# Kernel tuning notes

Hardware: AMD Instinct MI355X
Metric: run time of the kernel (lower is better)

The kernel has to match this reference:

```python
import jax, jax.numpy as jnp
import numpy as np
import math

B, N, M, H = 4, 1024, 1024, 512
EPS = 1e-5


def _ln(x, g, b):
    m = jnp.mean(x, axis=-1, keepdims=True)
    v = jnp.mean((x - m) ** 2, axis=-1, keepdims=True)
    return (x - m) * jax.lax.rsqrt(v + EPS) * g + b


def _heads(x, h):
    b, s, Hh = x.shape
    return x.reshape(b, s, h, Hh // h).transpose(0, 2, 1, 3)  # [b,h,s,d]


def _merge(x):
    b, h, s, d = x.shape
    return x.transpose(0, 2, 1, 3).reshape(b, s, h * d)


def _sdpa(q, k, v):
    d = q.shape[-1]
    a = jax.nn.softmax(jnp.einsum('bhqd,bhkd->bhqk', q, k) / math.sqrt(d), axis=-1)
    return jnp.einsum('bhqk,bhkd->bhqd', a, v)


def _attn(key, value, query, Wk, Wv, Wq, Wf, bf, g, b, h):
    residual = query
    K = _heads(key @ Wk, h)
    V = _heads(value @ Wv, h)
    Q = _heads(query @ Wq, h)
    r = _merge(_sdpa(Q, K, V))
    r = jnp.concatenate([residual, r], axis=-1) @ Wf + bf
    return _ln(r + residual, g, b)


def _sc_attn(x, x2, Wk, Wv, Wq, Wf, bf, g, b, h=2):
    residual = x
    sK, sV, sQ = _heads(x @ Wk, h), _heads(x @ Wv, h), _heads(x @ Wq, h)
    cK, cV, cQ = _heads(x2 @ Wk, h), _heads(x2 @ Wv, h), _heads(x2 @ Wq, h)
    r = _sdpa(sQ, sK, sV) + _sdpa(cQ, cK, cV) + _sdpa(cQ, sK, sV) + _sdpa(sQ, cK, cV)
    r = _merge(r)
    r = jnp.concatenate([residual, r], axis=-1) @ Wf + bf
    return _ln(r + residual, g, b)


def _forward(context_x, context_y, target_x, in_W, in_b, cx_W, cx_b, tx_W, tx_b,
             sc_Wk, sc_Wv, sc_Wq, sc_Wf, sc_bf, sc_g, sc_b,
             ca_Wk, ca_Wv, ca_Wq, ca_Wf, ca_bf, ca_g, ca_b):
    bsz = context_x.shape[0]
    y = context_y.reshape(bsz, -1, 4, 2)
    proj = lambda yd: jnp.concatenate([context_x, yd], axis=-1) @ in_W + in_b
    e = proj(y[:, :, 0, :])
    e1 = proj(y[:, :, 1, :])
    e2 = proj(y[:, :, 2, :])
    e3 = proj(y[:, :, 3, :])
    # first self pass: key2/value2/query2 == current encoder_input
    for i in range(2):
        e = _sc_attn(e, e, sc_Wk[i], sc_Wv[i], sc_Wq[i], sc_Wf[i], sc_bf[i], sc_g[i], sc_b[i])
    for x2 in (e1, e2, e3):
        for i in range(2):
            e = _sc_attn(e, x2, sc_Wk[i], sc_Wv[i], sc_Wq[i], sc_Wf[i], sc_bf[i], sc_g[i], sc_b[i])
    q = target_x @ tx_W + tx_b
    k = context_x @ cx_W + cx_b
    for i in range(2):
        q = _attn(k, e, q, ca_Wk[i], ca_Wv[i], ca_Wq[i], ca_Wf[i], ca_bf[i], ca_g[i], ca_b[i], h=4)
    return q


def setup_inputs() -> dict:
    key = jax.random.key(0)
    ks = jax.random.split(key, 24)
    w = lambda i, shape, s: jax.random.normal(ks[i], shape, jnp.float32) * s
    return {
        'context_x': jax.random.normal(ks[0], (B, N, 1), jnp.float32),
        'context_y': jax.random.normal(ks[1], (B, N, 8), jnp.float32),
        'target_x': jax.random.normal(ks[2], (B, M, 1), jnp.float32),
        'in_W': w(3, (3, H), 0.5), 'in_b': jnp.zeros((H,), jnp.float32),
        'cx_W': w(4, (1, H), 0.5), 'cx_b': jnp.zeros((H,), jnp.float32),
        'tx_W': w(5, (1, H), 0.5), 'tx_b': jnp.zeros((H,), jnp.float32),
        'sc_Wk': w(6, (2, H, H), 0.03), 'sc_Wv': w(7, (2, H, H), 0.03), 'sc_Wq': w(8, (2, H, H), 0.03),
        'sc_Wf': w(9, (2, 2 * H, H), 0.03), 'sc_bf': jnp.zeros((2, H), jnp.float32),
        'sc_g': jnp.ones((2, H), jnp.float32), 'sc_b': jnp.zeros((2, H), jnp.float32),
        'ca_Wk': w(10, (2, H, H), 0.03), 'ca_Wv': w(11, (2, H, H), 0.03), 'ca_Wq': w(12, (2, H, H), 0.03),
        'ca_Wf': w(13, (2, 2 * H, H), 0.03), 'ca_bf': jnp.zeros((2, H), jnp.float32),
        'ca_g': jnp.ones((2, H), jnp.float32), 'ca_b': jnp.zeros((2, H), jnp.float32),
    }


def reference(context_x, context_y, target_x, in_W, in_b, cx_W, cx_b, tx_W, tx_b,
              sc_Wk, sc_Wv, sc_Wq, sc_Wf, sc_bf, sc_g, sc_b,
              ca_Wk, ca_Wv, ca_Wq, ca_Wf, ca_bf, ca_g, ca_b):
    return _forward(context_x, context_y, target_x, in_W, in_b, cx_W, cx_b, tx_W, tx_b,
                    sc_Wk, sc_Wv, sc_Wq, sc_Wf, sc_bf, sc_g, sc_b,
                    ca_Wk, ca_Wv, ca_Wq, ca_Wf, ca_bf, ca_g, ca_b)
```

## Files before the change

### kernel.cpp

```cpp
#include <hip/hip_runtime.h>

#define DEVINL __device__ __forceinline__

typedef short bf16x8 __attribute__((ext_vector_type(8)));
typedef float f32x4 __attribute__((ext_vector_type(4)));

DEVINL unsigned f2b(float f) {
  unsigned u = __float_as_uint(f);
  u = (u + 0x7FFFu + ((u >> 16) & 1u)) >> 16;
  return u & 0xFFFFu;
}
DEVINL uint4 pack8(const float* v) {
  uint4 u;
  u.x = f2b(v[0]) | (f2b(v[1]) << 16);
  u.y = f2b(v[2]) | (f2b(v[3]) << 16);
  u.z = f2b(v[4]) | (f2b(v[5]) << 16);
  u.w = f2b(v[6]) | (f2b(v[7]) << 16);
  return u;
}

DEVINL float4 block_sum4(float4 v, float4* sh) {
  const int lane = threadIdx.x & 63, wid = threadIdx.x >> 6;
#pragma unroll
  for (int o = 32; o; o >>= 1) {
    v.x += __shfl_down(v.x, o);
    v.y += __shfl_down(v.y, o);
    v.z += __shfl_down(v.z, o);
    v.w += __shfl_down(v.w, o);
  }
  __syncthreads();
  if (lane == 0) sh[wid] = v;
  __syncthreads();
  float4 a = sh[0], b = sh[1], c = sh[2], d = sh[3], r;
  r.x = a.x + b.x + c.x + d.x;
  r.y = a.y + b.y + c.y + d.y;
  r.z = a.z + b.z + c.z + d.z;
  r.w = a.w + b.w + c.w + d.w;
  return r;
}
DEVINL float block_sum1(float v, float* sh) {
  const int lane = threadIdx.x & 63, wid = threadIdx.x >> 6;
#pragma unroll
  for (int o = 32; o; o >>= 1) v += __shfl_down(v, o);
  __syncthreads();
  if (lane == 0) sh[wid] = v;
  __syncthreads();
  return sh[0] + sh[1] + sh[2] + sh[3];
}

__global__ __launch_bounds__(256) void tabproj9_kernel(
    const float* __restrict__ in_W, const float* __restrict__ in_b,
    const float* __restrict__ cx_W, const float* __restrict__ cx_b,
    const float* __restrict__ tx_W, const float* __restrict__ tx_b,
    const float* __restrict__ sWk, const float* __restrict__ sWv,
    const float* __restrict__ sWq, const float* __restrict__ aWk,
    const float* __restrict__ aWq, float* __restrict__ Ttab) {
  const int z = blockIdx.y;
  const float* V;
  const float* bias;
  const float* W;
  float* P;
  int nvec;
  float scl = 1.f;
  if (z < 6) {
    V = in_W; bias = in_b; nvec = 3;
    const int i = z / 3, wsel = z % 3;
    W = (wsel == 0 ? sWk : wsel == 1 ? sWv : sWq) + (size_t)i * 262144;
    P = Ttab + (size_t)z * 2048;
    if (wsel == 2) scl = 0.0625f;
  } else if (z < 8) {
    V = cx_W; bias = cx_b; nvec = 1;
    W = aWk + (size_t)(z - 6) * 262144;
    P = Ttab + 12288 + (size_t)(z - 6) * 1024;
  } else {
    V = tx_W; bias = tx_b; nvec = 1;
    W = aWq; P = Ttab + 14336; scl = 0.08838834764831845f;
  }
  __shared__ float4 sh4[4];
  const int j = blockIdx.x, tid = threadIdx.x;
  float acc[4] = {0.f, 0.f, 0.f, 0.f};
  for (int kk = tid; kk < 512; kk += 256) {
    const float w = W[(size_t)kk * 512 + j];
    for (int v = 0; v < nvec; ++v) acc[v] += V[(size_t)v * 512 + kk] * w;
    acc[3] += bias[kk] * w;
  }
  float4 packed = make_float4(acc[0], acc[1], acc[2], acc[3]);
  packed = block_sum4(packed, sh4);
  if (tid == 0) {
    const float vals[4] = {packed.x * scl, packed.y * scl, packed.z * scl, packed.w * scl};
    for (int v = 0; v < nvec; ++v) P[(size_t)v * 512 + j] = vals[v];
    P[(size_t)nvec * 512 + j] = vals[3];
  }
}

__global__ __launch_bounds__(256) void transpose_kvq_kernel(
    const float* __restrict__ sWk, const float* __restrict__ sWv,
    const float* __restrict__ sWq, const float* __restrict__ aWv,
    const float* __restrict__ aWq, unsigned short* __restrict__ Wkvqt0,
    unsigned short* __restrict__ aWvt0, unsigned short* __restrict__ aWqt1) {
  const int z = blockIdx.z;
  const float* src;
  unsigned short* dst;
  float scl = 1.f;
  if (z < 6) {
    const int i = z / 3, wsel = z % 3;
    src = (wsel == 0 ? sWk : wsel == 1 ? sWv : sWq) + (size_t)i * 262144;
    dst = Wkvqt0 + (size_t)i * 786432 + (size_t)wsel * 262144;
    if (wsel == 2) scl = 0.0625f;
  } else if (z < 8) {
    src = aWv + (size_t)(z - 6) * 262144;
    dst = aWvt0 + (size_t)(z - 6) * 262144;
  } else {
    src = aWq + 262144; dst = aWqt1; scl = 0.08838834764831845f;
  }
  __shared__ float tile[32][33];
  const int n0 = blockIdx.x * 32, k0 = blockIdx.y * 32;
  const int tx = threadIdx.x, ty = threadIdx.y;
#pragma unroll
  for (int r = 0; r < 4; ++r)
    tile[ty + 8 * r][tx] = src[(size_t)(k0 + ty + 8 * r) * 512 + n0 + tx];
  __syncthreads();
#pragma unroll
  for (int r = 0; r < 4; ++r)
    dst[(size_t)(n0 + ty + 8 * r) * 512 + k0 + tx] =
        (unsigned short)f2b(scl * tile[tx][ty + 8 * r]);
}

__global__ __launch_bounds__(256) void transpose_f_kernel(
    const float* __restrict__ sWf, const float* __restrict__ aWf,
    unsigned short* __restrict__ Wft0, unsigned short* __restrict__ aWft0) {
  const int z = blockIdx.z;
  const float* src = (z < 2 ? sWf + (size_t)z * 524288 : aWf + (size_t)(z - 2) * 524288);
  unsigned short* dst =
      (z < 2 ? Wft0 + (size_t)z * 524288 : aWft0 + (size_t)(z - 2) * 524288);
  __shared__ float tile[32][33];
  const int n0 = blockIdx.x * 32, k0 = blockIdx.y * 32;
  const int tx = threadIdx.x, ty = threadIdx.y;
#pragma unroll
  for (int r = 0; r < 4; ++r)
    tile[ty + 8 * r][tx] = src[(size_t)(k0 + ty + 8 * r) * 512 + n0 + tx];
  __syncthreads();
#pragma unroll
  for (int r = 0; r < 4; ++r)
    dst[(size_t)(n0 + ty + 8 * r) * 1024 + k0 + tx] =
        (unsigned short)f2b(tile[tx][ty + 8 * r]);
}

__global__ __launch_bounds__(256) void vtrans_frag_kernel(
    const float* __restrict__ V, int ld, int nh, int D,
    unsigned short* __restrict__ Vfr) {
  __shared__ float tile[32][33];
  const int s0 = blockIdx.x * 32, d0 = blockIdx.y * 32;
  const int bh = blockIdx.z;
  const int b = bh / nh, h = bh % nh;
  const int tx = threadIdx.x, ty = threadIdx.y;
  const float* src = V + ((size_t)b * 1024 + s0) * ld + h * D + d0;
#pragma unroll
  for (int r = 0; r < 4; ++r)
    tile[ty + 8 * r][tx] = src[(size_t)(ty + 8 * r) * ld + tx];
  __syncthreads();
  const int idx = ty * 32 + tx;
  if (idx < 128) {
    const int dj = idx & 31, sch = idx >> 5;
    float v[8];
#pragma unroll
    for (int jj = 0; jj < 8; ++jj) v[jj] = tile[sch * 8 + jj][dj];
    const uint4 u = pack8(v);
    const int sc = s0 >> 5;
    const int dtile = (d0 + dj) >> 4;
    const int lane = sch * 16 + (dj & 15);
    *(uint4*)(Vfr + ((size_t)(bh * 32 + sc) * (D / 16) + dtile) * 512 + lane * 8) = u;
  }
}

__global__ __launch_bounds__(256) void affine3_pack_kernel(
    const float* __restrict__ cx, const float* __restrict__ cy, int sel,
    const float* __restrict__ TK, const float* __restrict__ TV,
    const float* __restrict__ TQ, unsigned short* __restrict__ Kfr,
    unsigned short* __restrict__ Qbf, float* __restrict__ Vf) {
  const int row = blockIdx.x;
  const int b = row >> 10, s = row & 1023;
  const float x = cx[row];
  const float* y = cy + (size_t)row * 8 + 2 * sel;
  const float y0 = y[0], y1 = y[1];
  const int t = threadIdx.x;
  if (t < 128) {
    const bool isQ = t >= 64;
    const int c = t & 63;
    const int h = c >> 5;
    const int d0 = (c & 31) * 8;
    const float* T = isQ ? TQ : TK;
    float v[8];
#pragma unroll
    for (int j = 0; j < 8; ++j) {
      const int col = h * 256 + d0 + j;
      v[j] = x * T[col] + y0 * T[512 + col] + y1 * T[1024 + col] + T[1536 + col];
    }
    const uint4 u = pack8(v);
    const int bh = b * 2 + h;
    if (isQ) {
      *(uint4*)(Qbf + ((size_t)bh * 1024 + s) * 256 + d0) = u;
    } else {
      const int kc = d0 >> 5;
      const int lane = ((d0 & 31) >> 3) * 16 + (s & 15);
      *(uint4*)(Kfr + ((size_t)(bh * 8 + kc) * 64 + (s >> 4)) * 512 + lane * 8) = u;
    }
  } else {
    const int col0 = (t - 128) * 4;
    float4 o;
    float* op = (float*)&o;
#pragma unroll
    for (int j = 0; j < 4; ++j) {
      const int col = col0 + j;
      op[j] = x * TV[col] + y0 * TV[512 + col] + y1 * TV[1024 + col] + TV[1536 + col];
    }
    *(float4*)(Vf + (size_t)row * 512 + col0) = o;
  }
}

__global__ __launch_bounds__(64) void rank1_pack_kernel(
    const float* __restrict__ x, const float* __restrict__ T,
    unsigned short* __restrict__ dst, int isQ) {
  const int row = blockIdx.x;
  const int b = row >> 10, s = row & 1023;
  const float xv = x[row];
  const int c = threadIdx.x;
  const int h = c >> 4;
  const int d0 = (c & 15) * 8;
  float v[8];
#pragma unroll
  for (int j = 0; j < 8; ++j) {
    const int col = h * 128 + d0 + j;
    v[j] = xv * T[col] + T[512 + col];
  }
  const uint4 u = pack8(v);
  const int bh = b * 4 + h;
  if (isQ) {
    *(uint4*)(dst + ((size_t)bh * 1024 + s) * 128 + d0) = u;
  } else {
    const int kc = d0 >> 5;
    const int lane = ((d0 & 31) >> 3) * 16 + (s & 15);
    *(uint4*)(dst + ((size_t)(bh * 4 + kc) * 64 + (s >> 4)) * 512 + lane * 8) = u;
  }
}

__global__ __launch_bounds__(512) void affine3_kernel(
    const float* __restrict__ cx, const float* __restrict__ cy, int sel,
    const float* __restrict__ W3, const float* __restrict__ bias,
    float* __restrict__ out, unsigned short* __restrict__ outb) {
  const int r = blockIdx.x, j = threadIdx.x;
  const float* y = cy + (size_t)r * 8 + 2 * sel;
  const float v = cx[r] * W3[j] + y[0] * W3[512 + j] + y[1] * W3[1024 + j] + bias[j];
  if (out) out[(size_t)r * 512 + j] = v;
  if (outb) outb[(size_t)r * 512 + j] = (unsigned short)f2b(v);
}

__global__ __launch_bounds__(512) void rank1_kernel(
    const float* __restrict__ x, const float* __restrict__ w,
    const float* __restrict__ b, float* __restrict__ out,
    unsigned short* __restrict__ outb) {
  const int r = blockIdx.x, j = threadIdx.x;
  const float v = x[r] * w[j] + b[j];
  if (out) out[(size_t)r * 512 + j] = v;
  if (outb) outb[(size_t)r * 512 + j] = (unsigned short)f2b(v);
}

__global__ __launch_bounds__(256) void gemm_wf_kernel(
    const unsigned short* __restrict__ A0, const unsigned short* __restrict__ A1,
    const float* __restrict__ F0, const float* __restrict__ F1,
    const unsigned short* __restrict__ Wt, const float* __restrict__ bias,
    float* __restrict__ C0, float* __restrict__ C1) {
  constexpr int BM = 128, BN = 64, BK = 32, LDP = 40, K = 512, N = 512;
  __shared__ unsigned short As[2][BM * LDP];
  __shared__ unsigned short Bs[2][BN * LDP];
  const int kz = blockIdx.z;
  const int tid = threadIdx.x;
  const int lane = tid & 63, w = tid >> 6;
  const int bm = blockIdx.y * BM, bn = blockIdx.x * BN;
  const int wm = (w & 1) * 64, wn = (w >> 1) * 32;
  const int l15 = lane & 15, lq = lane >> 4;
  const int ar = tid >> 1, ac = (tid & 1) * 16;
  const int br = tid >> 2, bc = (tid & 3) * 8;
  const unsigned short* A = kz ? A1 : A0;
  const bool useF = (kz != 0) && (F0 != nullptr);
  const size_t arow = (size_t)(bm + ar) * 512;
  const size_t brow = (size_t)(bn + br) * 1024 + (size_t)kz * 512;
  f32x4 acc[4][2] = {};
  uint4 ra0, ra1, rb0;
#define GLOAD(k0_)                                                          \
  do {                                                                      \
    if (useF) {                                                             \
      const float* p0 = F0 + arow + (k0_) + ac;                             \
      const float* p1 = F1 + arow + (k0_) + ac;                             \
      float s[16];                                                          \
      const float4 x0 = *(const float4*)p0, x1 = *(const float4*)(p0 + 4);  \
      const float4 x2 = *(const float4*)(p0 + 8), x3 = *(const float4*)(p0 + 12); \
      const float4 y0 = *(const float4*)p1, y1 = *(const float4*)(p1 + 4);  \
      const float4 y2 = *(const float4*)(p1 + 8), y3 = *(const float4*)(p1 + 12); \
      s[0] = x0.x + y0.x; s[1] = x0.y + y0.y; s[2] = x0.z + y0.z; s[3] = x0.w + y0.w; \
      s[4] = x1.x + y1.x; s[5] = x1.y + y1.y; s[6] = x1.z + y1.z; s[7] = x1.w + y1.w; \
      s[8] = x2.x + y2.x; s[9] = x2.y + y2.y; s[10] = x2.z + y2.z; s[11] = x2.w + y2.w; \
      s[12] = x3.x + y3.x; s[13] = x3.y + y3.y; s[14] = x3.z + y3.z; s[15] = x3.w + y3.w; \
      ra0 = pack8(s); ra1 = pack8(s + 8);                                   \
    } else {                                                                \
      ra0 = *(const uint4*)(A + arow + (k0_) + ac);                         \
      ra1 = *(const uint4*)(A + arow + (k0_) + ac + 8);                     \
    }                                                                       \
    rb0 = *(const uint4*)(Wt + brow + (k0_) + bc);                          \
  } while (0)
  GLOAD(0);
  *(uint4*)(As[0] + ar * LDP + ac) = ra0;
  *(uint4*)(As[0] + ar * LDP + ac + 8) = ra1;
  *(uint4*)(Bs[0] + br * LDP + bc) = rb0;
  __syncthreads();
  int buf = 0;
  for (int k0 = 0; k0 < K; k0 += BK) {
    const bool more = (k0 + BK) < K;
    if (more) GLOAD(k0 + BK);
    bf16x8 af[4], bfr[2];
#pragma unroll
    for (int mt = 0; mt < 4; ++mt)
      af[mt] = *(const bf16x8*)(As[buf] + (wm + mt * 16 + l15) * LDP + lq * 8);
#pragma unroll
    for (int nt = 0; nt < 2; ++nt)
      bfr[nt] = *(const bf16x8*)(Bs[buf] + (wn + nt * 16 + l15) * LDP + lq * 8);
#pragma unroll
    for (int mt = 0; mt < 4; ++mt)
#pragma unroll
      for (int nt = 0; nt < 2; ++nt)
        acc[mt][nt] =
            __builtin_amdgcn_mfma_f32_16x16x32_bf16(af[mt], bfr[nt], acc[mt][nt], 0, 0, 0);
    if (more) {
      *(uint4*)(As[buf ^ 1] + ar * LDP + ac) = ra0;
      *(uint4*)(As[buf ^ 1] + ar * LDP + ac + 8) = ra1;
      *(uint4*)(Bs[buf ^ 1] + br * LDP + bc) = rb0;
    }
    __syncthreads();
    buf ^= 1;
  }
#undef GLOAD
  float* C = kz ? C1 : C0;
#pragma unroll
  for (int nt = 0; nt < 2; ++nt) {
    const int col = bn + wn + nt * 16 + l15;
    const float bv = (kz && bias) ? bias[col] : 0.f;
#pragma unroll
    for (int mt = 0; mt < 4; ++mt) {
#pragma unroll
      for (int r = 0; r < 4; ++r) {
        const int row = bm + wm + mt * 16 + lq * 4 + r;
        C[(size_t)row * N + col] = acc[mt][nt][r] + bv;
      }
    }
  }
}

template <int MODE>
__global__ __launch_bounds__(256) void gemm_pack_kernel(
    const unsigned short* __restrict__ A0, const unsigned short* __restrict__ Wt,
    unsigned short* __restrict__ Kfr, unsigned short* __restrict__ Vfr,
    unsigned short* __restrict__ Qbf) {
  constexpr int BM = 128, BN = 64, BK = 32, LDP = 40, K = 512;
  __shared__ unsigned short As[2][BM * LDP];
  __shared__ unsigned short Bs[2][BN * LDP];
  const int tid = threadIdx.x;
  const int lane = tid & 63, w = tid >> 6;
  const int bm = blockIdx.y * BM, bn = blockIdx.x * BN;
  const int wm = (w & 1) * 64, wn = (w >> 1) * 32;
  const int l15 = lane & 15, lq = lane >> 4;
  const int ar = tid >> 1, ac = (tid & 1) * 16;
  const int br = tid >> 2, bc = (tid & 3) * 8;
  f32x4 acc[4][2] = {};
  uint4 ra0 = *(const uint4*)(A0 + (size_t)(bm + ar) * K + ac);
  uint4 ra1 = *(const uint4*)(A0 + (size_t)(bm + ar) * K + ac + 8);
  uint4 rb0 = *(const uint4*)(Wt + (size_t)(bn + br) * K + bc);
  *(uint4*)(As[0] + ar * LDP + ac) = ra0;
  *(uint4*)(As[0] + ar * LDP + ac + 8) = ra1;
  *(uint4*)(Bs[0] + br * LDP + bc) = rb0;
  __syncthreads();
  int buf = 0;
  for (int k0 = 0; k0 < K; k0 += BK) {
    const bool more = (k0 + BK) < K;
    if (more) {
      ra0 = *(const uint4*)(A0 + (size_t)(bm + ar) * K + k0 + BK + ac);
      ra1 = *(const uint4*)(A0 + (size_t)(bm + ar) * K + k0 + BK + ac + 8);
      rb0 = *(const uint4*)(Wt + (size_t)(bn + br) * K + k0 + BK + bc);
    }
    bf16x8 af[4], bfr[2];
#pragma unroll
    for (int mt = 0; mt < 4; ++mt)
      af[mt] = *(const bf16x8*)(As[buf] + (wm + mt * 16 + l15) * LDP + lq * 8);
#pragma unroll
    for (int nt = 0; nt < 2; ++nt)
      bfr[nt] = *(const bf16x8*)(Bs[buf] + (wn + nt * 16 + l15) * LDP + lq * 8);
#pragma unroll
    for (int mt = 0; mt < 4; ++mt)
#pragma unroll
      for (int nt = 0; nt < 2; ++nt)
        acc[mt][nt] =
            __builtin_amdgcn_mfma_f32_16x16x32_bf16(af[mt], bfr[nt], acc[mt][nt], 0, 0, 0);
    if (more) {
      *(uint4*)(As[buf ^ 1] + ar * LDP + ac) = ra0;
      *(uint4*)(As[buf ^ 1] + ar * LDP + ac + 8) = ra1;
      *(uint4*)(Bs[buf ^ 1] + br * LDP + bc) = rb0;
    }
    __syncthreads();
    buf ^= 1;
  }
  const int b = bm >> 10;
  const int s0base = (bm & 1023) + wm + lq * 4;
#pragma unroll
  for (int nt = 0; nt < 2; ++nt) {
    const int col = bn + wn + nt * 16 + l15;
    int sec, h, d, nh2, Dv;
    if constexpr (MODE == 0) {
      sec = col >> 9; const int c = col & 511; h = c >> 8; d = c & 255; nh2 = 2; Dv = 256;
    } else if constexpr (MODE == 1) {
      sec = 1; h = col >> 7; d = col & 127; nh2 = 4; Dv = 128;
    } else {
      sec = 2; h = col >> 7; d = col & 127; nh2 = 4; Dv = 128;
    }
    const int bh = b * nh2 + h;
#pragma unroll
    for (int mt = 0; mt < 4; ++mt) {
      const int s0 = s0base + mt * 16;
      const float* a = (const float*)&acc[mt][nt];
      if (sec == 2) {
        unsigned short* q = Qbf + ((size_t)bh * 1024 + s0) * Dv + d;
#pragma unroll
        for (int r = 0; r < 4; ++r) q[(size_t)r * Dv] = (unsigned short)f2b(a[r]);
      } else if (sec == 0) {
        unsigned short* kp = Kfr +
            ((size_t)(bh * 8 + (d >> 5)) * 64 + (s0 >> 4)) * 512 +
            ((d & 31) >> 3) * 128 + (d & 7);
#pragma unroll
        for (int r = 0; r < 4; ++r)
          kp[((s0 & 15) + r) * 8] = (unsigned short)f2b(a[r]);
      } else {
        unsigned short* vp = Vfr +
            ((size_t)(bh * 32 + (s0 >> 5)) * (Dv / 16) + (d >> 4)) * 512 +
            (((s0 >> 3) & 3) * 16 + (d & 15)) * 8 + (s0 & 7);
        uint2 u;
        u.x = f2b(a[0]) | (f2b(a[1]) << 16);
        u.y = f2b(a[2]) | (f2b(a[3]) << 16);
        *(uint2*)vp = u;
      }
    }
  }
}

template <int D, int NKV>
__global__ __launch_bounds__(256, 2) void attn_mfma_kernel(
    const unsigned short* __restrict__ Qa, const unsigned short* __restrict__ Qb,
    const unsigned short* __restrict__ KfrA, const unsigned short* __restrict__ KfrB,
    const unsigned short* __restrict__ VfrA, const unsigned short* __restrict__ VfrB,
    float post_scale, int nh, unsigned short* __restrict__ R,
    float* __restrict__ Rp) {
  constexpr int NQS = NKV;
  constexpr int QP = D + 8;
  constexpr int WP = 1024 + 8;
  constexpr int DT = D / 64;
  const int tid = threadIdx.x;
  const int lane = tid & 63, w = tid >> 6;
  const int l15 = lane & 15, lq = lane >> 4;
  const int nbh = 4 * nh;
  int bx = blockIdx.x;
  int side = 0;
  if constexpr (NKV == 2) { side = bx >> 9; bx &= 511; }
  const int bh = bx % nbh;
  const int qb16 = (bx / nbh) * 16;
  const int b = bh / nh, head = bh % nh;
  const size_t rowb = (size_t)b * 1024;
  const int colo = head * D;

  __shared__ unsigned short qsh[NQS * 16 * QP];
  __shared__ unsigned short wsh[16 * WP];
  __shared__ float redA[4][16];
  __shared__ float redB[4][16];

  for (int idx = tid; idx < NQS * 16 * (D / 8); idx += 256) {
    const int st = idx / (16 * (D / 8));
    const int rem = idx - st * 16 * (D / 8);
    const int r = rem / (D / 8), ch = rem - r * (D / 8);
    const unsigned short* Q = st ? Qb : Qa;
    const uint4 u = *(const uint4*)(Q + ((size_t)bh * 1024 + qb16 + r) * D + ch * 8);
    *(uint4*)(qsh + st * 16 * QP + r * QP + ch * 8) = u;
  }
  __syncthreads();

  const unsigned short* Kp = (side ? KfrB : KfrA) + (size_t)bh * ((size_t)D * 1024);
  const unsigned short* Vp = (side ? VfrB : VfrA) + (size_t)bh * ((size_t)D * 1024);

  f32x4 acc[NQS][16] = {};
#pragma unroll 1
  for (int kc = 0; kc < D / 32; ++kc) {
    bf16x8 kf[16];
#pragma unroll
    for (int st = 0; st < 16; ++st)
      kf[st] = *(const bf16x8*)(Kp + ((size_t)kc * 64 + w * 16 + st) * 512 + lane * 8);
    const bf16x8 qa = *(const bf16x8*)(qsh + l15 * QP + kc * 32 + lq * 8);
    __builtin_amdgcn_s_setprio(1);
#pragma unroll
    for (int st = 0; st < 16; ++st)
      acc[0][st] = __builtin_amdgcn_mfma_f32_16x16x32_bf16(qa, kf[st], acc[0][st], 0, 0, 0);
    __builtin_amdgcn_s_setprio(0);
    if constexpr (NQS == 2) {
      const bf16x8 qb2 = *(const bf16x8*)(qsh + 16 * QP + l15 * QP + kc * 32 + lq * 8);
      __builtin_amdgcn_s_setprio(1);
#pragma unroll
      for (int st = 0; st < 16; ++st)
        acc[1][st] =
            __builtin_amdgcn_mfma_f32_16x16x32_bf16(qb2, kf[st], acc[1][st], 0, 0, 0);
      __builtin_amdgcn_s_setprio(0);
    }
  }

  float psA[4] = {0.f, 0.f, 0.f, 0.f}, psB[4] = {0.f, 0.f, 0.f, 0.f};
#pragma unroll
  for (int st = 0; st < 16; ++st)
#pragma unroll
    for (int r = 0; r < 4; ++r) {
      acc[0][st][r] = __expf(acc[0][st][r]);
      psA[r] += acc[0][st][r];
      if constexpr (NQS == 2) {
        acc[1][st][r] = __expf(acc[1][st][r]);
        psB[r] += acc[1][st][r];
      }
    }
#pragma unroll
  for (int o = 1; o < 16; o <<= 1)
#pragma unroll
    for (int r = 0; r < 4; ++r) {
      psA[r] += __shfl_xor(psA[r], o);
      if constexpr (NQS == 2) psB[r] += __shfl_xor(psB[r], o);
    }
  if (l15 == 0) {
#pragma unroll
    for (int r = 0; r < 4; ++r) {
      redA[w][lq * 4 + r] = psA[r];
      if constexpr (NQS == 2) redB[w][lq * 4 + r] = psB[r];
    }
  }
  __syncthreads();
  float invA[4], invB[4];
#pragma unroll
  for (int r = 0; r < 4; ++r) {
    invA[r] = 1.f / (redA[0][lq * 4 + r] + redA[1][lq * 4 + r] +
                     redA[2][lq * 4 + r] + redA[3][lq * 4 + r]);
    if constexpr (NQS == 2)
      invB[r] = 1.f / (redB[0][lq * 4 + r] + redB[1][lq * 4 + r] +
                       redB[2][lq * 4 + r] + redB[3][lq * 4 + r]);
  }
#pragma unroll
  for (int st = 0; st < 16; ++st)
#pragma unroll
    for (int r = 0; r < 4; ++r) {
      float wv = acc[0][st][r] * invA[r];
      if constexpr (NQS == 2) wv += acc[1][st][r] * invB[r];
      wsh[(lq * 4 + r) * WP + w * 256 + st * 16 + l15] = (unsigned short)f2b(wv);
    }
  __syncthreads();

  f32x4 acc_o[DT] = {};
#pragma unroll 1
  for (int sc = 0; sc < 32; sc += 2) {
    bf16x8 pa[2], vb[2][DT];
#pragma unroll
    for (int u = 0; u < 2; ++u) {
      pa[u] = *(const bf16x8*)(wsh + l15 * WP + (sc + u) * 32 + lq * 8);
#pragma unroll
      for (int dt = 0; dt < DT; ++dt)
        vb[u][dt] = *(const bf16x8*)(
            Vp + ((size_t)(sc + u) * (D / 16) + w * DT + dt) * 512 + lane * 8);
    }
    __builtin_amdgcn_s_setprio(1);
#pragma unroll
    for (int u = 0; u < 2; ++u)
#pragma unroll
      for (int dt = 0; dt < DT; ++dt)
        acc_o[dt] =
            __builtin_amdgcn_mfma_f32_16x16x32_bf16(pa[u], vb[u][dt], acc_o[dt], 0, 0, 0);
    __builtin_amdgcn_s_setprio(0);
  }

  if constexpr (NKV == 2) {
    float* dst = Rp + (size_t)side * (4096 * 512) + (rowb + qb16) * 512 + colo;
#pragma unroll
    for (int dt = 0; dt < DT; ++dt)
#pragma unroll
      for (int r = 0; r < 4; ++r) {
        const int q = lq * 4 + r;
        const int d = w * (DT * 16) + dt * 16 + l15;
        dst[(size_t)q * 512 + d] = acc_o[dt][r];
      }
  } else {
#pragma unroll
    for (int dt = 0; dt < DT; ++dt)
#pragma unroll
      for (int r = 0; r < 4; ++r) {
        const int q = lq * 4 + r;
        const int d = w * (DT * 16) + dt * 16 + l15;
        R[(rowb + qb16 + q) * 512 + colo + d] =
            (unsigned short)f2b(acc_o[dt][r] * post_scale);
      }
  }
}

__global__ __launch_bounds__(256) void ln_kernel(
    const float* __restrict__ G0, const float* __restrict__ G1,
    const float* __restrict__ res, const float* __restrict__ g,
    const float* __restrict__ b, float* __restrict__ out,
    unsigned short* __restrict__ outb) {
  __shared__ float sh[4];
  const int row = blockIdx.x, tid = threadIdx.x;
  const size_t off = (size_t)row * 512;
  const float x0 = G0[off + tid] + G1[off + tid] + res[off + tid];
  const float x1 = G0[off + tid + 256] + G1[off + tid + 256] + res[off + tid + 256];
  const float mean = block_sum1(x0 + x1, sh) * (1.0f / 512.0f);
  const float d0 = x0 - mean, d1 = x1 - mean;
  const float var = block_sum1(d0 * d0 + d1 * d1, sh) * (1.0f / 512.0f);
  const float inv = rsqrtf(var + 1e-5f);
  const float y0 = d0 * inv * g[tid] + b[tid];
  const float y1 = d1 * inv * g[tid + 256] + b[tid + 256];
  out[off + tid] = y0;
  out[off + tid + 256] = y1;
  if (outb) {
    outb[off + tid] = (unsigned short)f2b(y0);
    outb[off + tid + 256] = (unsigned short)f2b(y1);
  }
}

extern "C" void kernel_launch(void* const* d_in, const int* in_sizes, int n_in,
                              void* d_out, int out_size, void* d_ws, size_t ws_size,
                              hipStream_t stream) {
  typedef unsigned short ushort_t;
  const float* cx   = (const float*)d_in[0];
  const float* cy   = (const float*)d_in[1];
  const float* txp  = (const float*)d_in[2];
  const float* in_W = (const float*)d_in[3];
  const float* in_b = (const float*)d_in[4];
  const float* cx_W = (const float*)d_in[5];
  const float* cx_b = (const float*)d_in[6];
  const float* tx_W = (const float*)d_in[7];
  const float* tx_b = (const float*)d_in[8];
  const float* sWk  = (const float*)d_in[9];
  const float* sWv  = (const float*)d_in[10];
  const float* sWq  = (const float*)d_in[11];
  const float* sWf  = (const float*)d_in[12];
  const float* sbf  = (const float*)d_in[13];
  const float* sg   = (const float*)d_in[14];
  const float* sb   = (const float*)d_in[15];
  const float* aWk  = (const float*)d_in[16];
  const float* aWv  = (const float*)d_in[17];
  const float* aWq  = (const float*)d_in[18];
  const float* aWf  = (const float*)d_in[19];
  const float* abf  = (const float*)d_in[20];
  const float* ag   = (const float*)d_in[21];
  const float* ab   = (const float*)d_in[22];

  const size_t MB = 1024 * 1024;
  char* ws = (char*)d_ws;
  float*    E     = (float*)(ws + 0 * MB);
  ushort_t* Ebf   = (ushort_t*)(ws + 8 * MB);
  float*    QA    = (float*)(ws + 12 * MB);
  ushort_t* QAbf  = (ushort_t*)(ws + 20 * MB);
  ushort_t* Rbbf  = (ushort_t*)(ws + 24 * MB);
  float*    Rp    = (float*)(ws + 28 * MB);
  float*    G0    = (float*)(ws + 44 * MB);
  ushort_t* KfrA  = (ushort_t*)(ws + 52 * MB);
  ushort_t* VfrA  = (ushort_t*)(ws + 56 * MB);
  ushort_t* QbfA  = (ushort_t*)(ws + 60 * MB);
  ushort_t* KfrB  = (ushort_t*)(ws + 64 * MB);
  ushort_t* VfrB  = (ushort_t*)(ws + 68 * MB);
  ushort_t* QbfB  = (ushort_t*)(ws + 72 * MB);
  float*    cVf   = (float*)(ws + 76 * MB);
  float*    G1    = (float*)(ws + 84 * MB);
  ushort_t* Wkvqt0 = (ushort_t*)(ws + 92 * MB);
  ushort_t* Wkvqt[2] = {Wkvqt0, Wkvqt0 + 786432};
  ushort_t* Wft0   = (ushort_t*)(ws + 95 * MB);
  ushort_t* Wft[2] = {Wft0, Wft0 + 524288};
  ushort_t* aWvt0  = (ushort_t*)(ws + 97 * MB);
  ushort_t* aWvt[2] = {aWvt0, aWvt0 + 262144};
  ushort_t* aWqt1  = (ushort_t*)(ws + 98 * MB);
  ushort_t* aWft0  = (ushort_t*)(ws + 99 * MB);
  ushort_t* aWft[2] = {aWft0, aWft0 + 524288};
  float*    Ttab   = (float*)(ws + 101 * MB);

  float* T_sc[2][3];
  for (int i = 0; i < 2; ++i)
    for (int w = 0; w < 3; ++w) T_sc[i][w] = Ttab + (size_t)(i * 3 + w) * 2048;
  float* T_cak[2] = {Ttab + 12288, Ttab + 12288 + 1024};
  float* T_caq0 = Ttab + 14336;

  const dim3 tb(32, 8);

  transpose_kvq_kernel<<<dim3(16, 16, 9), tb, 0, stream>>>(sWk, sWv, sWq, aWv, aWq,
                                                           Wkvqt0, aWvt0, aWqt1);
  transpose_f_kernel<<<dim3(16, 32, 4), tb, 0, stream>>>(sWf, aWf, Wft0, aWft0);
  tabproj9_kernel<<<dim3(512, 9), 256, 0, stream>>>(in_W, in_b, cx_W, cx_b, tx_W, tx_b,
                                                    sWk, sWv, sWq, aWk, aWq, Ttab);

  affine3_kernel<<<4096, 512, 0, stream>>>(cx, cy, 0, in_W, in_b, E, Ebf);
  rank1_kernel<<<4096, 512, 0, stream>>>(txp, tx_W, tx_b, QA, QAbf);

  for (int p = 0; p < 4; ++p) {
    for (int i = 0; i < 2; ++i) {
      gemm_pack_kernel<0><<<dim3(24, 32), 256, 0, stream>>>(Ebf, Wkvqt[i], KfrA, VfrA,
                                                            QbfA);
      const float* F0 = nullptr;
      const float* F1 = nullptr;
      if (p > 0) {
        affine3_pack_kernel<<<4096, 256, 0, stream>>>(cx, cy, p, T_sc[i][0], T_sc[i][1],
                                                      T_sc[i][2], KfrB, QbfB, cVf);
        vtrans_frag_kernel<<<dim3(32, 8, 8), tb, 0, stream>>>(cVf, 512, 2, 256, VfrB);
        attn_mfma_kernel<256, 2><<<1024, 256, 0, stream>>>(
            QbfA, QbfB, KfrA, KfrB, VfrA, VfrB, 1.0f, 2, nullptr, Rp);
        F0 = Rp; F1 = Rp + 4096 * 512;
      } else {
        attn_mfma_kernel<256, 1><<<512, 256, 0, stream>>>(
            QbfA, QbfA, KfrA, KfrA, VfrA, VfrA, 4.0f, 2, Rbbf, nullptr);
      }
      gemm_wf_kernel<<<dim3(8, 32, 2), 256, 0, stream>>>(
          Ebf, Rbbf, F0, F1, Wft[i], sbf + (size_t)i * 512, G0, G1);
      ln_kernel<<<4096, 256, 0, stream>>>(G0, G1, E, sg + (size_t)i * 512,
                                          sb + (size_t)i * 512, E, Ebf);
    }
  }

  for (int i = 0; i < 2; ++i) {
    rank1_pack_kernel<<<4096, 64, 0, stream>>>(cx, T_cak[i], KfrA, 0);
    gemm_pack_kernel<1><<<dim3(8, 32), 256, 0, stream>>>(Ebf, aWvt[i], nullptr, VfrA,
                                                         nullptr);
    if (i == 0) {
      rank1_pack_kernel<<<4096, 64, 0, stream>>>(txp, T_caq0, QbfB, 1);
    } else {
      gemm_pack_kernel<2><<<dim3(8, 32), 256, 0, stream>>>(QAbf, aWqt1, nullptr, nullptr,
                                                           QbfB);
    }
    attn_mfma_kernel<128, 1><<<1024, 256, 0, stream>>>(
        QbfB, QbfB, KfrA, KfrA, VfrA, VfrA, 1.0f, 4, Rbbf, nullptr);
    gemm_wf_kernel<<<dim3(8, 32, 2), 256, 0, stream>>>(
        QAbf, Rbbf, nullptr, nullptr, aWft[i], abf + (size_t)i * 512, G0, G1);
    ln_kernel<<<4096, 256, 0, stream>>>(G0, G1, QA, ag + (size_t)i * 512,
                                        ab + (size_t)i * 512,
                                        (i == 1) ? (float*)d_out : QA,
                                        (i == 1) ? nullptr : QAbf);
  }
  (void)in_sizes; (void)n_in; (void)out_size; (void)ws_size;
}
```

Baseline: 1.060 ms.

## Fuse V affine into fragment packing, use exp2 softmax, halve attention weight smem

Folds log2(e) into the Q scaling so the softmax can use exp2f instead of __expf. Replaces the affine3_pack plus vtrans_frag pair with a K/Q affine kernel and a V kernel that computes the affine values directly into the fragment layout, which removes the fp32 V intermediate round-trip through global memory. The attention kernel now stages probability weights through half-sized shared memory in two passes. That lowers LDS use and may raise occupancy, but adds extra barriers and a remapped V chunk index.

Measured after the change: 1.592 ms. +50.2%, slower.

```diff
diff --git a/kernel.cpp b/kernel.cpp
--- a/kernel.cpp
+++ b/kernel.cpp
@@ -4,6 +4,8 @@
 
 typedef short bf16x8 __attribute__((ext_vector_type(8)));
 typedef float f32x4 __attribute__((ext_vector_type(4)));
+
+#define LOG2E 1.44269504088896f
 
 DEVINL unsigned f2b(float f) {
   unsigned u = __float_as_uint(f);
@@ -67,14 +69,14 @@
     const int i = z / 3, wsel = z % 3;
     W = (wsel == 0 ? sWk : wsel == 1 ? sWv : sWq) + (size_t)i * 262144;
     P = Ttab + (size_t)z * 2048;
-    if (wsel == 2) scl = 0.0625f;
+    if (wsel == 2) scl = 0.0625f * LOG2E;
   } else if (z < 8) {
     V = cx_W; bias = cx_b; nvec = 1;
     W = aWk + (size_t)(z - 6) * 262144;
     P = Ttab + 12288 + (size_t)(z - 6) * 1024;
   } else {
     V = tx_W; bias = tx_b; nvec = 1;
-    W = aWq; P = Ttab + 14336; scl = 0.08838834764831845f;
+    W = aWq; P = Ttab + 14336; scl = 0.08838834764831845f * LOG2E;
   }
   __shared__ float4 sh4[4];
   const int j = blockIdx.x, tid = threadIdx.x;
@@ -106,12 +108,12 @@
     const int i = z / 3, wsel = z % 3;
     src = (wsel == 0 ? sWk : wsel == 1 ? sWv : sWq) + (size_t)i * 262144;
     dst = Wkvqt0 + (size_t)i * 786432 + (size_t)wsel * 262144;
-    if (wsel == 2) scl = 0.0625f;
+    if (wsel == 2) scl = 0.0625f * LOG2E;
   } else if (z < 8) {
     src = aWv + (size_t)(z - 6) * 262144;
     dst = aWvt0 + (size_t)(z - 6) * 262144;
   } else {
-    src = aWq + 262144; dst = aWqt1; scl = 0.08838834764831845f;
+    src = aWq + 262144; dst = aWqt1; scl = 0.08838834764831845f * LOG2E;
   }
   __shared__ float tile[32][33];
   const int n0 = blockIdx.x * 32, k0 = blockIdx.y * 32;
@@ -146,75 +148,68 @@
         (unsigned short)f2b(tile[tx][ty + 8 * r]);
 }
 
-__global__ __launch_bounds__(256) void vtrans_frag_kernel(
-    const float* __restrict__ V, int ld, int nh, int D,
-    unsigned short* __restrict__ Vfr) {
-  __shared__ float tile[32][33];
-  const int s0 = blockIdx.x * 32, d0 = blockIdx.y * 32;
-  const int bh = blockIdx.z;
-  const int b = bh / nh, h = bh % nh;
-  const int tx = threadIdx.x, ty = threadIdx.y;
-  const float* src = V + ((size_t)b * 1024 + s0) * ld + h * D + d0;
-#pragma unroll
-  for (int r = 0; r < 4; ++r)
-    tile[ty + 8 * r][tx] = src[(size_t)(ty + 8 * r) * ld + tx];
-  __syncthreads();
-  const int idx = ty * 32 + tx;
-  if (idx < 128) {
-    const int dj = idx & 31, sch = idx >> 5;
-    float v[8];
-#pragma unroll
-    for (int jj = 0; jj < 8; ++jj) v[jj] = tile[sch * 8 + jj][dj];
-    const uint4 u = pack8(v);
-    const int sc = s0 >> 5;
-    const int dtile = (d0 + dj) >> 4;
-    const int lane = sch * 16 + (dj & 15);
-    *(uint4*)(Vfr + ((size_t)(bh * 32 + sc) * (D / 16) + dtile) * 512 + lane * 8) = u;
-  }
-}
-
-__global__ __launch_bounds__(256) void affine3_pack_kernel(
+__global__ __launch_bounds__(128) void affine3kq_kernel(
     const float* __restrict__ cx, const float* __restrict__ cy, int sel,
-    const float* __restrict__ TK, const float* __restrict__ TV,
-    const float* __restrict__ TQ, unsigned short* __restrict__ Kfr,
-    unsigned short* __restrict__ Qbf, float* __restrict__ Vf) {
+    const float* __restrict__ TK, const float* __restrict__ TQ,
+    unsigned short* __restrict__ Kfr, unsigned short* __restrict__ Qbf) {
   const int row = blockIdx.x;
   const int b = row >> 10, s = row & 1023;
   const float x = cx[row];
   const float* y = cy + (size_t)row * 8 + 2 * sel;
   const float y0 = y[0], y1 = y[1];
   const int t = threadIdx.x;
-  if (t < 128) {
-    const bool isQ = t >= 64;
-    const int c = t & 63;
-    const int h = c >> 5;
-    const int d0 = (c & 31) * 8;
-    const float* T = isQ ? TQ : TK;
+  const bool isQ = t >= 64;
+  const int c = t & 63;
+  const int h = c >> 5;
+  const int d0 = (c & 31) * 8;
+  const float* T = isQ ? TQ : TK;
+  float v[8];
+#pragma unroll
+  for (int j = 0; j < 8; ++j) {
+    const int col = h * 256 + d0 + j;
+    v[j] = x * T[col] + y0 * T[512 + col] + y1 * T[1024 + col] + T[1536 + col];
+  }
+  const uint4 u = pack8(v);
+  const int bh = b * 2 + h;
+  if (isQ) {
+    *(uint4*)(Qbf + ((size_t)bh * 1024 + s) * 256 + d0) = u;
+  } else {
+    const int kc = d0 >> 5;
+    const int lane = ((d0 & 31) >> 3) * 16 + (s & 15);
+    *(uint4*)(Kfr + ((size_t)(bh * 8 + kc) * 64 + (s >> 4)) * 512 + lane * 8) = u;
+  }
+}
+
+__global__ __launch_bounds__(256) void affine3v_frag_kernel(
+    const float* __restrict__ cx, const float* __restrict__ cy, int sel,
+    const float* __restrict__ TV, unsigned short* __restrict__ Vfr) {
+  __shared__ float tile[32][33];
+  const int s0 = blockIdx.x * 32, d0 = blockIdx.y * 32;
+  const int bh = blockIdx.z;
+  const int b = bh >> 1, h = bh & 1;
+  const int tx = threadIdx.x, ty = threadIdx.y;
+  const int col = h * 256 + d0 + tx;
+  const float tv0 = TV[col], tv1 = TV[512 + col], tv2 = TV[1024 + col],
+              tv3 = TV[1536 + col];
+#pragma unroll
+  for (int r = 0; r < 4; ++r) {
+    const int row = b * 1024 + s0 + ty + 8 * r;
+    const float x = cx[row];
+    const float* y = cy + (size_t)row * 8 + 2 * sel;
+    tile[ty + 8 * r][tx] = x * tv0 + y[0] * tv1 + y[1] * tv2 + tv3;
+  }
+  __syncthreads();
+  const int idx = ty * 32 + tx;
+  if (idx < 128) {
+    const int dj = idx & 31, sch = idx >> 5;
     float v[8];
 #pragma unroll
-    for (int j = 0; j < 8; ++j) {
-      const int col = h * 256 + d0 + j;
-      v[j] = x * T[col] + y0 * T[512 + col] + y1 * T[1024 + col] + T[1536 + col];
-    }
+    for (int jj = 0; jj < 8; ++jj) v[jj] = tile[sch * 8 + jj][dj];
     const uint4 u = pack8(v);
-    const int bh = b * 2 + h;
-    if (isQ) {
-      *(uint4*)(Qbf + ((size_t)bh * 1024 + s) * 256 + d0) = u;
-    } else {
-      const int kc = d0 >> 5;
-      const int lane = ((d0 & 31) >> 3) * 16 + (s & 15);
-      *(uint4*)(Kfr + ((size_t)(bh * 8 + kc) * 64 + (s >> 4)) * 512 + lane * 8) = u;
-    }
-  } else {
-    const int col0 = (t - 128) * 4;
-    float4 o;
-    float* op = (float*)&o;
-#pragma unroll
-    for (int j = 0; j < 4; ++j) {
-      const int col = col0 + j;
-      op[j] = x * TV[col] + y0 * TV[512 + col] + y1 * TV[1024 + col] + TV[1536 + col];
-    }
-    *(float4*)(Vf + (size_t)row * 512 + col0) = o;
+    const int sc = s0 >> 5;
+    const int dtile = (d0 + dj) >> 4;
+    const int lane = sch * 16 + (dj & 15);
+    *(uint4*)(Vfr + ((size_t)(bh * 32 + sc) * 16 + dtile) * 512 + lane * 8) = u;
   }
 }
 
@@ -458,7 +453,7 @@
     float* __restrict__ Rp) {
   constexpr int NQS = NKV;
   constexpr int QP = D + 8;
-  constexpr int WP = 1024 + 8;
+  constexpr int WPh = 512 + 8;
   constexpr int DT = D / 64;
   const int tid = threadIdx.x;
   const int lane = tid & 63, w = tid >> 6;
@@ -474,7 +469,7 @@
   const int colo = head * D;
 
   __shared__ unsigned short qsh[NQS * 16 * QP];
-  __shared__ unsigned short wsh[16 * WP];
+  __shared__ unsigned short wsh[16 * WPh];
   __shared__ float redA[4][16];
   __shared__ float redB[4][16];
 
@@ -520,10 +515,10 @@
   for (int st = 0; st < 16; ++st)
 #pragma unroll
     for (int r = 0; r < 4; ++r) {
-      acc[0][st][r] = __expf(acc[0][st][r]);
+      acc[0][st][r] = exp2f(acc[0][st][r]);
       psA[r] += acc[0][st][r];
       if constexpr (NQS == 2) {
-        acc[1][st][r] = __expf(acc[1][st][r]);
+        acc[1][st][r] = exp2f(acc[1][st][r]);
         psB[r] += acc[1][st][r];
       }
     }
@@ -551,36 +546,44 @@
       invB[r] = 1.f / (redB[0][lq * 4 + r] + redB[1][lq * 4 + r] +
                        redB[2][lq * 4 + r] + redB[3][lq * 4 + r]);
   }
-#pragma unroll
-  for (int st = 0; st < 16; ++st)
-#pragma unroll
-    for (int r = 0; r < 4; ++r) {
-      float wv = acc[0][st][r] * invA[r];
-      if constexpr (NQS == 2) wv += acc[1][st][r] * invB[r];
-      wsh[(lq * 4 + r) * WP + w * 256 + st * 16 + l15] = (unsigned short)f2b(wv);
-    }
-  __syncthreads();
 
   f32x4 acc_o[DT] = {};
 #pragma unroll 1
-  for (int sc = 0; sc < 32; sc += 2) {
-    bf16x8 pa[2], vb[2][DT];
-#pragma unroll
-    for (int u = 0; u < 2; ++u) {
-      pa[u] = *(const bf16x8*)(wsh + l15 * WP + (sc + u) * 32 + lq * 8);
-#pragma unroll
-      for (int dt = 0; dt < DT; ++dt)
-        vb[u][dt] = *(const bf16x8*)(
-            Vp + ((size_t)(sc + u) * (D / 16) + w * DT + dt) * 512 + lane * 8);
-    }
-    __builtin_amdgcn_s_setprio(1);
-#pragma unroll
-    for (int u = 0; u < 2; ++u)
-#pragma unroll
-      for (int dt = 0; dt < DT; ++dt)
-        acc_o[dt] =
-            __builtin_amdgcn_mfma_f32_16x16x32_bf16(pa[u], vb[u][dt], acc_o[dt], 0, 0, 0);
-    __builtin_amdgcn_s_setprio(0);
+  for (int half = 0; half < 2; ++half) {
+#pragma unroll
+    for (int st = 0; st < 8; ++st) {
+      const int g = half * 8 + st;
+#pragma unroll
+      for (int r = 0; r < 4; ++r) {
+        float wv = acc[0][g][r] * invA[r];
+        if constexpr (NQS == 2) wv += acc[1][g][r] * invB[r];
+        wsh[(lq * 4 + r) * WPh + w * 128 + st * 16 + l15] = (unsigned short)f2b(wv);
+      }
+    }
+    __syncthreads();
+#pragma unroll 1
+    for (int sh2 = 0; sh2 < 16; sh2 += 2) {
+      bf16x8 pa[2], vb[2][DT];
+#pragma unroll
+      for (int u = 0; u < 2; ++u) {
+        const int sc = sh2 + u;
+        pa[u] = *(const bf16x8*)(wsh + l15 * WPh + sc * 32 + lq * 8);
+        const int scg = (sc >> 2) * 8 + half * 4 + (sc & 3);
+#pragma unroll
+        for (int dt = 0; dt < DT; ++dt)
+          vb[u][dt] = *(const bf16x8*)(
+              Vp + ((size_t)scg * (D / 16) + w * DT + dt) * 512 + lane * 8);
+      }
+      __builtin_amdgcn_s_setprio(1);
+#pragma unroll
+      for (int u = 0; u < 2; ++u)
+#pragma unroll
+        for (int dt = 0; dt < DT; ++dt)
+          acc_o[dt] =
+              __builtin_amdgcn_mfma_f32_16x16x32_bf16(pa[u], vb[u][dt], acc_o[dt], 0, 0, 0);
+      __builtin_amdgcn_s_setprio(0);
+    }
+    __syncthreads();
   }
 
   if constexpr (NKV == 2) {
@@ -673,7 +676,6 @@
   ushort_t* KfrB  = (ushort_t*)(ws + 64 * MB);
   ushort_t* VfrB  = (ushort_t*)(ws + 68 * MB);
   ushort_t* QbfB  = (ushort_t*)(ws + 72 * MB);
-  float*    cVf   = (float*)(ws + 76 * MB);
   float*    G1    = (float*)(ws + 84 * MB);
   ushort_t* Wkvqt0 = (ushort_t*)(ws + 92 * MB);
   ushort_t* Wkvqt[2] = {Wkvqt0, Wkvqt0 + 786432};
@@ -710,9 +712,10 @@
       const float* F0 = nullptr;
       const float* F1 = nullptr;
       if (p > 0) {
-        affine3_pack_kernel<<<4096, 256, 0, stream>>>(cx, cy, p, T_sc[i][0], T_sc[i][1],
-                                                      T_sc[i][2], KfrB, QbfB, cVf);
-        vtrans_frag_kernel<<<dim3(32, 8, 8), tb, 0, stream>>>(cVf, 512, 2, 256, VfrB);
+        affine3kq_kernel<<<4096, 128, 0, stream>>>(cx, cy, p, T_sc[i][0], T_sc[i][2],
+                                                   KfrB, QbfB);
+        affine3v_frag_kernel<<<dim3(32, 8, 8), tb, 0, stream>>>(cx, cy, p, T_sc[i][1],
+                                                                VfrB);
         attn_mfma_kernel<256, 2><<<1024, 256, 0, stream>>>(
             QbfA, QbfB, KfrA, KfrB, VfrA, VfrB, 1.0f, 2, nullptr, Rp);
         F0 = Rp; F1 = Rp + 4096 * 512;
```
